# Kernel tuning notes

Measured on AMD Instinct MI355X. Metric: run time of the kernel, lower is better.

Reference implementation:

```python
import jax, jax.numpy as jnp
import numpy as np

K = 64        # number of negative samples (init arg k)
MARGIN = 1.0  # init arg margin
CHUNK = 128   # anchor chunk size for the L1 cdist (bounds peak memory)


def l1_cdist(X, Y):
    """Pairwise L1 distances [A, N] computed in CHUNK-row slabs to avoid a [A, N, d] blowup."""
    A, d = X.shape
    Xc = X.reshape(A // CHUNK, CHUNK, d)
    f = lambda xc: jnp.sum(jnp.abs(xc[:, None, :] - Y[None, :, :]), axis=-1)  # [CHUNK, N]
    return jax.lax.map(f, Xc).reshape(A, Y.shape[0])


def setup_inputs() -> dict:
    key = jax.random.key(0)
    k1, k2, k3, k4, k5 = jax.random.split(key, 5)
    N1 = N2 = 8192
    D = 128
    A = 1024
    out1 = jax.random.normal(k1, (N1, D), dtype=jnp.float32)
    out2 = jax.random.normal(k2, (N2, D), dtype=jnp.float32)
    ot_cost = jax.random.uniform(k5, (N1, N2), dtype=jnp.float32)
    anchor1 = jax.random.randint(k3, (A,), 0, N1)
    anchor2 = jax.random.randint(k4, (A,), 0, N2)
    return {"out1": out1, "out2": out2, "ot_cost": ot_cost,
            "anchor1": anchor1, "anchor2": anchor2}


def reference(out1, out2, ot_cost, anchor1, anchor2):
    a1 = out1[anchor1]  # [A, d]
    a2 = out2[anchor2]  # [A, d]

    # Negative sampling: k nearest (by L1) nodes in the other graph to each anchor.
    # Indices are integer-valued, so (like the torch detach/numpy path) no grad flows here.
    d1 = l1_cdist(a1, out2)               # [A, N2]
    neg1 = jnp.argsort(d1, axis=1)[:, :K]  # [A, K]
    d2 = l1_cdist(a2, out1)               # [A, N1]
    neg2 = jnp.argsort(d2, axis=1)[:, :K]  # [A, K]

    # OT-cost weighting of the negative embeddings.
    w1 = ot_cost[anchor1[:, None], neg1]      # [A, K]
    w2 = ot_cost.T[anchor2[:, None], neg2]    # [A, K]
    n1 = out2[neg1] * w1[..., None]           # [A, K, d]
    n2 = out1[neg2] * w2[..., None]           # [A, K, d]

    # Margin ranking loss with L1 distances.
    pos = jnp.sum(jnp.abs(a1 - a2), axis=1)           # [A]
    Dm = pos + MARGIN                                  # [A]
    B1 = -jnp.sum(jnp.abs(a1[:, None, :] - n1), -1)    # [A, K]
    B2 = -jnp.sum(jnp.abs(a2[:, None, :] - n2), -1)    # [A, K]
    L1 = jnp.sum(jax.nn.relu(Dm[:, None] + B1))
    L2 = jnp.sum(jax.nn.relu(Dm[:, None] + B2))
    return (L1 + L2) / (anchor1.shape[0] * K)
```

## Files before the change

kernel.cpp:

```cpp
#include <hip/hip_runtime.h>
#include <hip/hip_bf16.h>
#include <cstdint>

#define NPTS 8192
#define DIM  128
#define NA   1024
#define KSEL 64

#define AS1 __attribute__((address_space(1)))
#define AS3 __attribute__((address_space(3)))

typedef unsigned short ushort_t;
typedef __fp16 h2v __attribute__((ext_vector_type(2)));

__device__ __forceinline__ uint32_t pkcvt(float x, float y) {
  h2v h = __builtin_amdgcn_cvt_pkrtz(x, y);
  return __builtin_bit_cast(uint32_t, h);
}
__device__ __forceinline__ void dot2a(float& a, uint32_t m, uint32_t o) {
  asm("v_dot2_f32_f16 %0, %1, %2, %0" : "+v"(a) : "v"(m), "v"(o));
}
__device__ __forceinline__ uint32_t pkmax(uint32_t a, uint32_t b) {
  uint32_t d;
  asm("v_pk_max_f16 %0, %1, %2" : "=v"(d) : "v"(a), "v"(b));
  return d;
}

__global__ __launch_bounds__(256)
void convert_kernel(const float* __restrict__ out1, const float* __restrict__ out2,
                    ushort_t* __restrict__ h1, ushort_t* __restrict__ h2,
                    float* __restrict__ S1, float* __restrict__ S2) {
  const int t    = threadIdx.x;
  const int side = blockIdx.x >> 10;
  const int row  = (blockIdx.x & 1023) * 8 + (t >> 5);
  const int lane = t & 31;

  uint32_t ones;
  asm("v_mov_b32 %0, 0x3C003C00" : "=v"(ones));

  const float* src = (side ? out2 : out1) + (size_t)row * DIM + lane * 4;
  ushort_t* dsth   = (side ? h2 : h1) + (size_t)row * DIM + lane * 4;
  float4 v = *(const float4*)src;
  uint2 u;
  u.x = pkcvt(v.x, v.y);
  u.y = pkcvt(v.z, v.w);
  *(uint2*)dsth = u;

  float s = 0.f;
  dot2a(s, u.x, ones);
  dot2a(s, u.y, ones);
#pragma unroll
  for (int o = 16; o; o >>= 1) s += __shfl_xor(s, o);
  if (lane == 0) (side ? S2 : S1)[row] = s;
}

#define BM 128
#define BN 128

__global__ __launch_bounds__(256)
void dist_kernel(const ushort_t* __restrict__ h1, const ushort_t* __restrict__ h2,
                 const int* __restrict__ anchor1, const int* __restrict__ anchor2,
                 const float* __restrict__ S1, const float* __restrict__ S2,
                 ushort_t* __restrict__ Dmat) {
  __shared__ alignas(16) char Ah[2][8192];
  __shared__ alignas(16) char Bh[2][8192];

  const int t = threadIdx.x;
  int bid = blockIdx.x;
  bid = (bid & 7) * 128 + (bid >> 3);
  const int mt  = bid & 15;
  const int nt  = bid >> 4;
  const int dir = mt >> 3;
  const int i0  = (mt & 7) * BM;
  const int j0  = nt * BN;

  const ushort_t* __restrict__ Ah16 = dir ? h2 : h1;
  const ushort_t* __restrict__ Bh16 = dir ? h1 : h2;
  const float* __restrict__ SA = dir ? S2 : S1;
  const float* __restrict__ SB = dir ? S1 : S2;
  const int* __restrict__ anc  = dir ? anchor2 : anchor1;

  const int srow = t & 127;
  const int p0   = t >> 7;
  const int arow = anc[i0 + srow];
  uint32_t offA[2], offB[2];
#pragma unroll
  for (int q = 0; q < 2; ++q) {
    const int plane = p0 + 2 * q;
    offA[q] = (uint32_t)arow * DIM + plane * 8;
    offB[q] = (uint32_t)(j0 + srow) * DIM + plane * 8;
  }

  const int ty = t >> 4;
  const int tx = t & 15;

  float acc[8][8];
#pragma unroll
  for (int r = 0; r < 8; ++r)
#pragma unroll
    for (int c = 0; c < 8; ++c) acc[r][c] = 0.f;

  uint32_t ones;
  asm("v_mov_b32 %0, 0x3C003C00" : "=v"(ones));

#define STAGE(BUF, KT)                                                         \
  {                                                                            \
    _Pragma("unroll")                                                          \
    for (int q = 0; q < 2; ++q) {                                              \
      __builtin_amdgcn_global_load_lds(                                        \
          (const AS1 uint32_t*)(Ah16 + offA[q] + (KT) * 32),                   \
          (AS3 uint32_t*)(&Ah[BUF][t * 16 + q * 4096]), 16, 0, 0);             \
      __builtin_amdgcn_global_load_lds(                                        \
          (const AS1 uint32_t*)(Bh16 + offB[q] + (KT) * 32),                   \
          (AS3 uint32_t*)(&Bh[BUF][t * 16 + q * 4096]), 16, 0, 0);             \
    }                                                                          \
  }

  STAGE(0, 0)

#pragma unroll 1
  for (int kt = 0; kt < 4; ++kt) {
    __builtin_amdgcn_s_barrier();
    if (kt < 3) {
      STAGE((kt + 1) & 1, kt + 1)
      asm volatile("s_waitcnt vmcnt(4)" ::: "memory");
    } else {
      asm volatile("s_waitcnt vmcnt(0)" ::: "memory");
    }
    __builtin_amdgcn_s_barrier();
    __builtin_amdgcn_sched_barrier(0);

    const char* const Ab = &Ah[kt & 1][0] + ty * 16;
    const char* const Bb = &Bh[kt & 1][0] + tx * 16;

#pragma unroll 1
    for (int kc = 0; kc < 4; ++kc) {
      uint4 bv[8];
#pragma unroll
      for (int c = 0; c < 8; ++c)
        bv[c] = *(const uint4*)(Bb + kc * 2048 + c * 256);
      uint4 av = *(const uint4*)(Ab + kc * 2048);
#pragma unroll
      for (int r = 0; r < 8; ++r) {
        uint4 avn = av;
        if (r < 7) avn = *(const uint4*)(Ab + kc * 2048 + (r + 1) * 256);
#pragma unroll
        for (int c = 0; c < 8; ++c) {
          dot2a(acc[r][c], pkmax(av.x, bv[c].x), ones);
          dot2a(acc[r][c], pkmax(av.y, bv[c].y), ones);
          dot2a(acc[r][c], pkmax(av.z, bv[c].z), ones);
          dot2a(acc[r][c], pkmax(av.w, bv[c].w), ones);
        }
        av = avn;
      }
    }
  }

#undef STAGE

  float sa[8], sb[8];
#pragma unroll
  for (int r = 0; r < 8; ++r) sa[r] = SA[anc[i0 + r * 16 + ty]];
#pragma unroll
  for (int c = 0; c < 8; ++c) sb[c] = SB[j0 + c * 16 + tx];

#pragma unroll
  for (int r = 0; r < 8; ++r) {
    ushort_t* dst = Dmat + (size_t)(dir * NA + i0 + r * 16 + ty) * NPTS + j0 + tx;
#pragma unroll
    for (int c = 0; c < 8; ++c) {
      float d = 2.f * acc[r][c] - sa[r] - sb[c];
      dst[c * 16] = (ushort_t)pkcvt(d, 0.f);
    }
  }
}

__global__ __launch_bounds__(256, 4)
void select_loss_kernel(const float* __restrict__ out1, const float* __restrict__ out2,
                        const float* __restrict__ ot,
                        const int* __restrict__ anchor1, const int* __restrict__ anchor2,
                        const ushort_t* __restrict__ Dmat, float* __restrict__ partials) {
  __shared__ ushort_t sdh[NPTS];
  __shared__ float a_self[DIM];
  __shared__ float terms[KSEL];
  __shared__ int   sel[KSEL];
  __shared__ unsigned wred[4];
  __shared__ float sm_pos;
  __shared__ int sm_cnt, sm_tie;

  const int t   = threadIdx.x;
  const int b   = blockIdx.x;
  const int dir = b >> 10;
  const int i   = b & (NA - 1);

  const int a1i = anchor1[i];
  const int a2i = anchor2[i];
  const int ai_self = dir ? a2i : a1i;
  const float* __restrict__ selfB = dir ? out2 : out1;
  const float* __restrict__ othB  = dir ? out1 : out2;

  const uint4* drow = (const uint4*)(Dmat + (size_t)b * NPTS);
#pragma unroll
  for (int q = 0; q < 4; ++q) ((uint4*)sdh)[t + q * 256] = drow[t + q * 256];

  if (t < 32) ((float4*)a_self)[t] = ((const float4*)(selfB + (size_t)ai_self * DIM))[t];

  if (t == 0) { sm_cnt = 0; sm_tie = 0; }

  if (t < 64) {
    const float* r1 = out1 + (size_t)a1i * DIM;
    const float* r2 = out2 + (size_t)a2i * DIM;
    float pz = fabsf(r1[t] - r2[t]) + fabsf(r1[t + 64] - r2[t + 64]);
#pragma unroll
    for (int o = 32; o; o >>= 1) pz += __shfl_down(pz, o);
    if (t == 0) sm_pos = pz;
  }
  __syncthreads();

  unsigned keys[32];
#pragma unroll
  for (int q = 0; q < 32; ++q) keys[q] = sdh[t + q * 256];

  unsigned lo = 0u, hi = 0x7C00u;
  while (lo < hi) {
    unsigned mid = lo + ((hi - lo) >> 1);
    unsigned c = 0;
#pragma unroll
    for (int q = 0; q < 32; ++q) c += (keys[q] <= mid) ? 1u : 0u;
#pragma unroll
    for (int o = 32; o; o >>= 1) c += __shfl_down(c, o);
    if ((t & 63) == 0) wred[t >> 6] = c;
    __syncthreads();
    c = wred[0] + wred[1] + wred[2] + wred[3];
    if (c >= 64u) hi = mid; else lo = mid + 1u;
    __syncthreads();
  }
  const unsigned T = lo;

  {
    unsigned c = 0;
#pragma unroll
    for (int q = 0; q < 32; ++q) c += (keys[q] < T) ? 1u : 0u;
#pragma unroll
    for (int o = 32; o; o >>= 1) c += __shfl_down(c, o);
    if ((t & 63) == 0) wred[t >> 6] = c;
  }
  __syncthreads();
  const int need = 64 - (int)(wred[0] + wred[1] + wred[2] + wred[3]);

#pragma unroll
  for (int q = 0; q < 32; ++q) {
    unsigned k = keys[q];
    bool take = false;
    if (k < T) take = true;
    else if (k == T) take = (atomicAdd(&sm_tie, 1) < need);
    if (take) {
      int s = atomicAdd(&sm_cnt, 1);
      sel[s] = t + q * 256;
    }
  }
  __syncthreads();

  {
    const int s  = t >> 2;
    const int tq = t & 3;
    const int j  = sel[s];
    const float w = dir ? ot[(size_t)j * NPTS + ai_self]
                        : ot[(size_t)ai_self * NPTS + j];
    const float* br = othB + (size_t)j * DIM;
    float dist = 0.f;
#pragma unroll
    for (int d = 0; d < 32; d += 4) {
      float4 bv = *(const float4*)(br + tq * 32 + d);
      dist += fabsf(a_self[tq * 32 + d + 0] - w * bv.x);
      dist += fabsf(a_self[tq * 32 + d + 1] - w * bv.y);
      dist += fabsf(a_self[tq * 32 + d + 2] - w * bv.z);
      dist += fabsf(a_self[tq * 32 + d + 3] - w * bv.w);
    }
    dist += __shfl_xor(dist, 1);
    dist += __shfl_xor(dist, 2);
    if (tq == 0) terms[s] = fmaxf(0.f, sm_pos + 1.0f - dist);
  }
  __syncthreads();

  if (t < 64) {
    float v = terms[t];
#pragma unroll
    for (int o = 32; o; o >>= 1) v += __shfl_down(v, o);
    if (t == 0) partials[b] = v;
  }
}

__global__ __launch_bounds__(256)
void reduce_kernel(const float* __restrict__ partials, float* __restrict__ outp) {
  __shared__ float ws4[4];
  const int t = threadIdx.x;
  float v = 0.f;
#pragma unroll
  for (int q = 0; q < 8; ++q) v += partials[t + q * 256];
#pragma unroll
  for (int o = 32; o; o >>= 1) v += __shfl_down(v, o);
  if ((t & 63) == 0) ws4[t >> 6] = v;
  __syncthreads();
  if (t == 0) outp[0] = (ws4[0] + ws4[1] + ws4[2] + ws4[3]) * (1.0f / 65536.0f);
}

extern "C" void kernel_launch(void* const* d_in, const int* in_sizes, int n_in,
                              void* d_out, int out_size, void* d_ws, size_t ws_size,
                              hipStream_t stream) {
  (void)in_sizes; (void)n_in; (void)out_size; (void)ws_size;
  const float* out1  = (const float*)d_in[0];
  const float* out2  = (const float*)d_in[1];
  const float* ot    = (const float*)d_in[2];
  const int* anchor1 = (const int*)d_in[3];
  const int* anchor2 = (const int*)d_in[4];

  char* ws = (char*)d_ws;
  ushort_t* Dmat  = (ushort_t*)ws;
  ushort_t* h1    = (ushort_t*)(ws + 33554432);
  ushort_t* h2    = (ushort_t*)(ws + 35651584);
  float* S1       = (float*)(ws + 37748736);
  float* S2       = (float*)(ws + 37781504);
  float* partials = (float*)(ws + 37814272);

  convert_kernel<<<dim3(2048), dim3(256), 0, stream>>>(out1, out2, h1, h2, S1, S2);
  dist_kernel<<<dim3(16 * 64), dim3(256), 0, stream>>>(h1, h2, anchor1, anchor2, S1, S2, Dmat);
  select_loss_kernel<<<dim3(2 * NA), dim3(256), 0, stream>>>(out1, out2, ot, anchor1, anchor2,
                                                             Dmat, partials);
  reduce_kernel<<<dim3(1), dim3(256), 0, stream>>>(partials, (float*)d_out);
}
```

Measured before the change: 120.4 us.

## Keep distance row in packed registers and tighten radix-select bisection bounds

The select kernel no longer stages the 8192-entry fp16 distance row in shared memory. Each thread now holds its slice as 16 packed 32-bit registers loaded straight from global memory. The bisection starts from the block-wide min and max key instead of the full fp16 range, which cuts the number of iterations. One barrier per iteration is dropped by double-buffering the reduction slots. Freeing the 16KB of LDS and removing the launch-bounds occupancy hint lets more blocks fit per CU, at the cost of a different element-to-thread mapping and possible register-pressure changes.

```diff
diff --git a/kernel.cpp b/kernel.cpp
--- a/kernel.cpp
+++ b/kernel.cpp
@@ -175,16 +175,17 @@
   }
 }
 
-__global__ __launch_bounds__(256, 4)
+__global__ __launch_bounds__(256)
 void select_loss_kernel(const float* __restrict__ out1, const float* __restrict__ out2,
                         const float* __restrict__ ot,
                         const int* __restrict__ anchor1, const int* __restrict__ anchor2,
                         const ushort_t* __restrict__ Dmat, float* __restrict__ partials) {
-  __shared__ ushort_t sdh[NPTS];
   __shared__ float a_self[DIM];
   __shared__ float terms[KSEL];
   __shared__ int   sel[KSEL];
-  __shared__ unsigned wred[4];
+  __shared__ unsigned wred[2][4];
+  __shared__ unsigned wless[4];
+  __shared__ unsigned wmin[4], wmax[4];
   __shared__ float sm_pos;
   __shared__ int sm_cnt, sm_tie;
 
@@ -199,14 +200,19 @@
   const float* __restrict__ selfB = dir ? out2 : out1;
   const float* __restrict__ othB  = dir ? out1 : out2;
 
-  const uint4* drow = (const uint4*)(Dmat + (size_t)b * NPTS);
-#pragma unroll
-  for (int q = 0; q < 4; ++q) ((uint4*)sdh)[t + q * 256] = drow[t + q * 256];
+  unsigned U[16];
+  {
+    const uint4* drow = (const uint4*)(Dmat + (size_t)b * NPTS);
+#pragma unroll
+    for (int q = 0; q < 4; ++q) {
+      uint4 k = drow[t + q * 256];
+      U[4 * q + 0] = k.x; U[4 * q + 1] = k.y;
+      U[4 * q + 2] = k.z; U[4 * q + 3] = k.w;
+    }
+  }
 
   if (t < 32) ((float4*)a_self)[t] = ((const float4*)(selfB + (size_t)ai_self * DIM))[t];
-
   if (t == 0) { sm_cnt = 0; sm_tie = 0; }
-
   if (t < 64) {
     const float* r1 = out1 + (size_t)a1i * DIM;
     const float* r2 = out2 + (size_t)a2i * DIM;
@@ -215,48 +221,73 @@
     for (int o = 32; o; o >>= 1) pz += __shfl_down(pz, o);
     if (t == 0) sm_pos = pz;
   }
-  __syncthreads();
-
-  unsigned keys[32];
-#pragma unroll
-  for (int q = 0; q < 32; ++q) keys[q] = sdh[t + q * 256];
-
-  unsigned lo = 0u, hi = 0x7C00u;
+
+  {
+    unsigned kmin = 0xFFFFu, kmax = 0u;
+#pragma unroll
+    for (int u = 0; u < 16; ++u) {
+      unsigned lo16 = U[u] & 0xFFFFu, hi16 = U[u] >> 16;
+      kmin = min(kmin, min(lo16, hi16));
+      kmax = max(kmax, max(lo16, hi16));
+    }
+#pragma unroll
+    for (int o = 32; o; o >>= 1) {
+      kmin = min(kmin, (unsigned)__shfl_xor((int)kmin, o));
+      kmax = max(kmax, (unsigned)__shfl_xor((int)kmax, o));
+    }
+    if ((t & 63) == 0) { wmin[t >> 6] = kmin; wmax[t >> 6] = kmax; }
+  }
+  __syncthreads();
+
+  unsigned lo = min(min(wmin[0], wmin[1]), min(wmin[2], wmin[3]));
+  unsigned hi = max(max(wmax[0], wmax[1]), max(wmax[2], wmax[3]));
+
+  int it = 0;
   while (lo < hi) {
-    unsigned mid = lo + ((hi - lo) >> 1);
+    const unsigned mid = lo + ((hi - lo) >> 1);
     unsigned c = 0;
 #pragma unroll
-    for (int q = 0; q < 32; ++q) c += (keys[q] <= mid) ? 1u : 0u;
+    for (int u = 0; u < 16; ++u) {
+      c += ((U[u] & 0xFFFFu) <= mid) ? 1u : 0u;
+      c += ((U[u] >> 16) <= mid) ? 1u : 0u;
+    }
 #pragma unroll
     for (int o = 32; o; o >>= 1) c += __shfl_down(c, o);
-    if ((t & 63) == 0) wred[t >> 6] = c;
+    if ((t & 63) == 0) wred[it & 1][t >> 6] = c;
     __syncthreads();
-    c = wred[0] + wred[1] + wred[2] + wred[3];
+    c = wred[it & 1][0] + wred[it & 1][1] + wred[it & 1][2] + wred[it & 1][3];
     if (c >= 64u) hi = mid; else lo = mid + 1u;
-    __syncthreads();
+    ++it;
   }
   const unsigned T = lo;
 
   {
     unsigned c = 0;
 #pragma unroll
-    for (int q = 0; q < 32; ++q) c += (keys[q] < T) ? 1u : 0u;
+    for (int u = 0; u < 16; ++u) {
+      c += ((U[u] & 0xFFFFu) < T) ? 1u : 0u;
+      c += ((U[u] >> 16) < T) ? 1u : 0u;
+    }
 #pragma unroll
     for (int o = 32; o; o >>= 1) c += __shfl_down(c, o);
-    if ((t & 63) == 0) wred[t >> 6] = c;
-  }
-  __syncthreads();
-  const int need = 64 - (int)(wred[0] + wred[1] + wred[2] + wred[3]);
-
-#pragma unroll
-  for (int q = 0; q < 32; ++q) {
-    unsigned k = keys[q];
-    bool take = false;
-    if (k < T) take = true;
-    else if (k == T) take = (atomicAdd(&sm_tie, 1) < need);
-    if (take) {
-      int s = atomicAdd(&sm_cnt, 1);
-      sel[s] = t + q * 256;
+    if ((t & 63) == 0) wless[t >> 6] = c;
+  }
+  __syncthreads();
+  const int need = 64 - (int)(wless[0] + wless[1] + wless[2] + wless[3]);
+
+#pragma unroll
+  for (int u = 0; u < 16; ++u) {
+    const int jbase = 8 * (t + (u >> 2) * 256) + 2 * (u & 3);
+#pragma unroll
+    for (int h = 0; h < 2; ++h) {
+      const unsigned k = h ? (U[u] >> 16) : (U[u] & 0xFFFFu);
+      bool take = false;
+      if (k < T) take = true;
+      else if (k == T) take = (atomicAdd(&sm_tie, 1) < need);
+      if (take) {
+        int s = atomicAdd(&sm_cnt, 1);
+        sel[s] = jbase + h;
+      }
     }
   }
   __syncthreads();
```

Result: faster. 110.1 us (-8.5%).
